# Kernel optimization log

Hardware: AMD Instinct MI355X
Metric: run time of the kernel (lower is better)

The kernel has to match this reference:

```python
import jax, jax.numpy as jnp
import numpy as np

B, F, V, E, A = 4096, 39, 100000, 16, 16


def setup_inputs() -> dict:
    key = jax.random.key(0)
    ks = jax.random.split(key, 9)
    Xi = jax.random.randint(ks[0], (B, F, 1), 0, V, dtype=jnp.int64)
    Xv = jax.random.uniform(ks[1], (B, F), dtype=jnp.float32)
    # stacked per-field embedding tables (all fields share vocab size V)
    emb1 = jax.random.normal(ks[2], (F, V, 1), dtype=jnp.float32) * 0.01   # first-order
    emb2 = jax.random.normal(ks[3], (F, V, E), dtype=jnp.float32) * 0.01   # second-order
    W1 = jax.random.normal(ks[4], (E, A), dtype=jnp.float32) * (1.0 / np.sqrt(E))
    b1 = jnp.zeros((A,), dtype=jnp.float32)
    H = jax.random.normal(ks[5], (A,), dtype=jnp.float32) * 0.2
    Pv = jax.random.normal(ks[6], (E,), dtype=jnp.float32) * 0.2
    bias = jax.random.normal(ks[7], (1,), dtype=jnp.float32) * 0.2
    return {"Xi": Xi, "Xv": Xv, "emb1": emb1, "emb2": emb2,
            "W1": W1, "b1": b1, "H": H, "Pv": Pv, "bias": bias}


def reference(Xi, Xv, emb1, emb2, W1, b1, H, Pv, bias):
    idx = Xi[..., 0]                      # [B, F] (sum over the size-1 index dim is identity)
    f = jnp.arange(idx.shape[1])
    # first-order: per-field scalar embedding * value -> [B, F]
    first = emb1[f[None, :], idx, 0] * Xv
    # second-order: per-field E-dim embedding * value -> [B, F, E]
    second = emb2[f[None, :], idx] * Xv[..., None]
    # pairwise elementwise products e_i * e_j for i<j -> [B, P, E], P = F*(F-1)/2
    ii, jj = np.triu_indices(idx.shape[1], k=1)
    wij = second[:, ii] * second[:, jj]
    # attention scoring (NOTE: source has activation commented out -> pure linear)
    att = jnp.einsum('bpe,ea->bpa', wij, W1) + b1          # [B, P, A]
    scores = jnp.einsum('bpa,a->bp', att, H)               # [B, P]
    attn_w = jax.nn.softmax(scores, axis=1)                # [B, P]
    att_out = jnp.einsum('bpe,e->bp', wij, Pv) * attn_w    # [B, P]
    return bias[0] + first.sum(axis=1) + att_out.sum(axis=1)  # [B]
```

## Files before the change

### kernel.cpp

```cpp
#include <hip/hip_runtime.h>
#include <math.h>


#define BB 4096
#define FF 39
#define VV 100000
#define EE 16
#define AA 16
#define PP (FF * (FF - 1) / 2)
#define SSTRIDE 20

__global__ __launch_bounds__(256) void afm_kernel(
    const int* __restrict__ Xi, const float* __restrict__ Xv,
    const float* __restrict__ emb1, const float* __restrict__ emb2,
    const float* __restrict__ W1, const float* __restrict__ b1,
    const float* __restrict__ H, const float* __restrict__ Pv,
    const float* __restrict__ bias, float* __restrict__ out)
{
    __shared__ float sec[FF * SSTRIDE];
    __shared__ float firstv[64];
    __shared__ float WHs[EE];
    __shared__ float PvS[EE];
    __shared__ short pairtab[PP];
    __shared__ float red[12];
    __shared__ float m_s;

    const int b = blockIdx.x;
    const int t = threadIdx.x;

    if (t < EE) {
        float s = 0.f;
#pragma unroll
        for (int a = 0; a < AA; ++a) s += W1[t * AA + a] * H[a];
        WHs[t] = s;
        PvS[t] = Pv[t];
    }
    if (t >= 64 && t < 128) firstv[t - 64] = 0.f;

    if (t < FF) {
        int base = t * (2 * FF - 1 - t) / 2;
        for (int j = t + 1; j < FF; ++j)
            pairtab[base + (j - t - 1)] = (short)((t << 8) | j);
    }

    if (t < FF * 4) {
        const int f = t >> 2, e4 = t & 3;
        const int idx = Xi[b * FF + f];
        const float xv = Xv[b * FF + f];
        const float4 v = *reinterpret_cast<const float4*>(
            emb2 + ((long)f * VV + idx) * EE + e4 * 4);
        float4 r;
        r.x = v.x * xv; r.y = v.y * xv; r.z = v.z * xv; r.w = v.w * xv;
        *reinterpret_cast<float4*>(&sec[f * SSTRIDE + e4 * 4]) = r;
    }

    if (t >= 192 && t < 192 + FF) {
        const int f = t - 192;
        const int idx = Xi[b * FF + f];
        firstv[f] = emb1[(long)f * VV + idx] * Xv[b * FF + f];
    }

    __syncthreads();

    float wh[EE], pv[EE];
#pragma unroll
    for (int e = 0; e < EE; ++e) { wh[e] = WHs[e]; pv[e] = PvS[e]; }

    float sv[3], qv[3];
    float local_max = -INFINITY;
#pragma unroll
    for (int k = 0; k < 3; ++k) {
        const int p = t + k * 256;
        float s = -INFINITY, q = 0.f;
        if (p < PP) {
            const int ij = pairtab[p];
            const int i = ij >> 8, j = ij & 255;
            const float4* __restrict__ si = reinterpret_cast<const float4*>(&sec[i * SSTRIDE]);
            const float4* __restrict__ sj = reinterpret_cast<const float4*>(&sec[j * SSTRIDE]);
            s = 0.f;
#pragma unroll
            for (int e4 = 0; e4 < 4; ++e4) {
                const float4 a = si[e4];
                const float4 c = sj[e4];
                const float w0 = a.x * c.x, w1 = a.y * c.y, w2 = a.z * c.z, w3 = a.w * c.w;
                s += w0 * wh[e4 * 4 + 0] + w1 * wh[e4 * 4 + 1]
                   + w2 * wh[e4 * 4 + 2] + w3 * wh[e4 * 4 + 3];
                q += w0 * pv[e4 * 4 + 0] + w1 * pv[e4 * 4 + 1]
                   + w2 * pv[e4 * 4 + 2] + w3 * pv[e4 * 4 + 3];
            }
            local_max = fmaxf(local_max, s);
        }
        sv[k] = s; qv[k] = q;
    }

    float m = local_max;
#pragma unroll
    for (int o = 32; o > 0; o >>= 1) m = fmaxf(m, __shfl_xor(m, o, 64));
    const int wid = t >> 6;
    if ((t & 63) == 0) red[wid] = m;
    __syncthreads();
    if (t == 0) m_s = fmaxf(fmaxf(red[0], red[1]), fmaxf(red[2], red[3]));
    __syncthreads();
    m = m_s;

    float den = 0.f, num = 0.f;
#pragma unroll
    for (int k = 0; k < 3; ++k) {
        const float e = __expf(sv[k] - m);
        den += e;
        num += e * qv[k];
    }
    float fs = (t < 64) ? firstv[t] : 0.f;
#pragma unroll
    for (int o = 32; o > 0; o >>= 1) {
        den += __shfl_xor(den, o, 64);
        num += __shfl_xor(num, o, 64);
        fs  += __shfl_xor(fs, o, 64);
    }
    if ((t & 63) == 0) { red[wid] = den; red[4 + wid] = num; red[8 + wid] = fs; }
    __syncthreads();
    if (t == 0) {
        const float D = red[0] + red[1] + red[2] + red[3];
        const float N = red[4] + red[5] + red[6] + red[7];
        out[b] = bias[0] + red[8] + N / D;
    }
}

extern "C" void kernel_launch(void* const* d_in, const int* in_sizes, int n_in,
                              void* d_out, int out_size, void* d_ws, size_t ws_size,
                              hipStream_t stream)
{
    const int*   Xi   = (const int*)d_in[0];
    const float* Xv   = (const float*)d_in[1];
    const float* emb1 = (const float*)d_in[2];
    const float* emb2 = (const float*)d_in[3];
    const float* W1   = (const float*)d_in[4];
    const float* b1   = (const float*)d_in[5];
    const float* H    = (const float*)d_in[6];
    const float* Pv   = (const float*)d_in[7];
    const float* bias = (const float*)d_in[8];
    (void)b1; (void)in_sizes; (void)n_in; (void)out_size; (void)d_ws; (void)ws_size;

    afm_kernel<<<BB, 256, 0, stream>>>(Xi, Xv, emb1, emb2, W1, b1, H, Pv, bias,
                                       (float*)d_out);
}
```

Baseline: 314.2 us.

## Use one wavefront per sample with online softmax over contiguous pair runs

Shrinks each block from 256 threads to a single 64-lane wavefront. Each lane walks 12 consecutive pairs, reusing the premultiplied i-row across j, and keeps an online softmax (running max, denominator, numerator). The partial results are merged with shuffle-only reductions, which removes the shared-memory reduction arrays and all but one barrier. This trades fewer threads per block and less gather parallelism for cheaper reductions and more row reuse. Each lane also does more serial work and uses more registers.

```diff
diff --git a/kernel.cpp b/kernel.cpp
--- a/kernel.cpp
+++ b/kernel.cpp
@@ -1,129 +1,136 @@
 #include <hip/hip_runtime.h>
 #include <math.h>
+#include <float.h>
 
 
 #define BB 4096
 #define FF 39
 #define VV 100000
 #define EE 16
-#define AA 16
-#define PP (FF * (FF - 1) / 2)
-#define SSTRIDE 20
+#define PP 741
+#define SS 20
 
-__global__ __launch_bounds__(256) void afm_kernel(
+__global__ __launch_bounds__(64) void afm_kernel(
     const int* __restrict__ Xi, const float* __restrict__ Xv,
     const float* __restrict__ emb1, const float* __restrict__ emb2,
-    const float* __restrict__ W1, const float* __restrict__ b1,
-    const float* __restrict__ H, const float* __restrict__ Pv,
-    const float* __restrict__ bias, float* __restrict__ out)
+    const float* __restrict__ W1, const float* __restrict__ H,
+    const float* __restrict__ Pv, const float* __restrict__ bias,
+    float* __restrict__ out)
 {
-    __shared__ float sec[FF * SSTRIDE];
-    __shared__ float firstv[64];
-    __shared__ float WHs[EE];
-    __shared__ float PvS[EE];
-    __shared__ short pairtab[PP];
-    __shared__ float red[12];
-    __shared__ float m_s;
+    __shared__ float sec[FF * SS];
 
     const int b = blockIdx.x;
-    const int t = threadIdx.x;
+    const int l = threadIdx.x;
 
-    if (t < EE) {
-        float s = 0.f;
-#pragma unroll
-        for (int a = 0; a < AA; ++a) s += W1[t * AA + a] * H[a];
-        WHs[t] = s;
-        PvS[t] = Pv[t];
-    }
-    if (t >= 64 && t < 128) firstv[t - 64] = 0.f;
-
-    if (t < FF) {
-        int base = t * (2 * FF - 1 - t) / 2;
-        for (int j = t + 1; j < FF; ++j)
-            pairtab[base + (j - t - 1)] = (short)((t << 8) | j);
+    int   xi = 0;
+    float xv = 0.f, fo = 0.f;
+    if (l < FF) {
+        xi = Xi[b * FF + l];
+        xv = Xv[b * FF + l];
+        fo = emb1[(long)l * VV + xi] * xv;
     }
 
-    if (t < FF * 4) {
-        const int f = t >> 2, e4 = t & 3;
-        const int idx = Xi[b * FF + f];
-        const float xv = Xv[b * FF + f];
-        const float4 v = *reinterpret_cast<const float4*>(
-            emb2 + ((long)f * VV + idx) * EE + e4 * 4);
-        float4 r;
-        r.x = v.x * xv; r.y = v.y * xv; r.z = v.z * xv; r.w = v.w * xv;
-        *reinterpret_cast<float4*>(&sec[f * SSTRIDE + e4 * 4]) = r;
+    const int e = l & 15;
+    float whe = 0.f;
+    {
+        const float4* __restrict__ W1r = reinterpret_cast<const float4*>(W1 + e * 16);
+        const float4* __restrict__ H4  = reinterpret_cast<const float4*>(H);
+#pragma unroll
+        for (int m = 0; m < 4; ++m) {
+            const float4 w = W1r[m], h = H4[m];
+            whe += w.x * h.x + w.y * h.y + w.z * h.z + w.w * h.w;
+        }
+    }
+    float wh[16];
+#pragma unroll
+    for (int k = 0; k < 16; ++k) wh[k] = __shfl(whe, k, 64);
+    float pv[16];
+    {
+        const float4* __restrict__ Pv4 = reinterpret_cast<const float4*>(Pv);
+#pragma unroll
+        for (int m = 0; m < 4; ++m) {
+            const float4 v = Pv4[m];
+            pv[m * 4 + 0] = v.x; pv[m * 4 + 1] = v.y;
+            pv[m * 4 + 2] = v.z; pv[m * 4 + 3] = v.w;
+        }
     }
 
-    if (t >= 192 && t < 192 + FF) {
-        const int f = t - 192;
-        const int idx = Xi[b * FF + f];
-        firstv[f] = emb1[(long)f * VV + idx] * Xv[b * FF + f];
+#pragma unroll
+    for (int k = 0; k < 3; ++k) {
+        const int t = l + 64 * k;
+        if (t < FF * 4) {
+            const int f = t >> 2, e4 = t & 3;
+            const int   idxf = __shfl(xi, f, 64);
+            const float xvf  = __shfl(xv, f, 64);
+            float4 v = *reinterpret_cast<const float4*>(
+                emb2 + ((long)f * VV + idxf) * EE + e4 * 4);
+            v.x *= xvf; v.y *= xvf; v.z *= xvf; v.w *= xvf;
+            *reinterpret_cast<float4*>(&sec[f * SS + e4 * 4]) = v;
+        }
+    }
+    __syncthreads();
+
+    const int p0  = l * 12;
+    const int cnt = (PP - p0 < 0) ? 0 : ((PP - p0 < 12) ? (PP - p0) : 12);
+    int rem = (p0 < PP) ? p0 : (PP - 1);
+    int i = 0;
+    while (rem >= FF - 1 - i) { rem -= FF - 1 - i; ++i; }
+    int j = i + 1 + rem;
+
+    float ui[16], ri[16];
+    auto load_i = [&](int ii) {
+#pragma unroll
+        for (int m = 0; m < 4; ++m) {
+            const float4 s4 = *reinterpret_cast<const float4*>(&sec[ii * SS + m * 4]);
+            ui[m * 4 + 0] = s4.x * wh[m * 4 + 0]; ri[m * 4 + 0] = s4.x * pv[m * 4 + 0];
+            ui[m * 4 + 1] = s4.y * wh[m * 4 + 1]; ri[m * 4 + 1] = s4.y * pv[m * 4 + 1];
+            ui[m * 4 + 2] = s4.z * wh[m * 4 + 2]; ri[m * 4 + 2] = s4.z * pv[m * 4 + 2];
+            ui[m * 4 + 3] = s4.w * wh[m * 4 + 3]; ri[m * 4 + 3] = s4.w * pv[m * 4 + 3];
+        }
+    };
+    load_i(i);
+
+    float mx = -FLT_MAX, den = 0.f, num = 0.f;
+#pragma unroll
+    for (int k = 0; k < 12; ++k) {
+        if (k < cnt) {
+            float s = 0.f, q = 0.f;
+#pragma unroll
+            for (int m = 0; m < 4; ++m) {
+                const float4 s4 = *reinterpret_cast<const float4*>(&sec[j * SS + m * 4]);
+                s += ui[m * 4 + 0] * s4.x + ui[m * 4 + 1] * s4.y
+                   + ui[m * 4 + 2] * s4.z + ui[m * 4 + 3] * s4.w;
+                q += ri[m * 4 + 0] * s4.x + ri[m * 4 + 1] * s4.y
+                   + ri[m * 4 + 2] * s4.z + ri[m * 4 + 3] * s4.w;
+            }
+            if (s > mx) {
+                const float sc = __expf(mx - s);
+                den *= sc; num *= sc; mx = s;
+            }
+            const float ex = __expf(s - mx);
+            den += ex;
+            num += ex * q;
+            if (++j == FF) {
+                ++i; j = i + 1;
+                if (k + 1 < cnt) load_i(i);
+            }
+        }
     }
 
-    __syncthreads();
-
-    float wh[EE], pv[EE];
 #pragma unroll
-    for (int e = 0; e < EE; ++e) { wh[e] = WHs[e]; pv[e] = PvS[e]; }
-
-    float sv[3], qv[3];
-    float local_max = -INFINITY;
-#pragma unroll
-    for (int k = 0; k < 3; ++k) {
-        const int p = t + k * 256;
-        float s = -INFINITY, q = 0.f;
-        if (p < PP) {
-            const int ij = pairtab[p];
-            const int i = ij >> 8, j = ij & 255;
-            const float4* __restrict__ si = reinterpret_cast<const float4*>(&sec[i * SSTRIDE]);
-            const float4* __restrict__ sj = reinterpret_cast<const float4*>(&sec[j * SSTRIDE]);
-            s = 0.f;
-#pragma unroll
-            for (int e4 = 0; e4 < 4; ++e4) {
-                const float4 a = si[e4];
-                const float4 c = sj[e4];
-                const float w0 = a.x * c.x, w1 = a.y * c.y, w2 = a.z * c.z, w3 = a.w * c.w;
-                s += w0 * wh[e4 * 4 + 0] + w1 * wh[e4 * 4 + 1]
-                   + w2 * wh[e4 * 4 + 2] + w3 * wh[e4 * 4 + 3];
-                q += w0 * pv[e4 * 4 + 0] + w1 * pv[e4 * 4 + 1]
-                   + w2 * pv[e4 * 4 + 2] + w3 * pv[e4 * 4 + 3];
-            }
-            local_max = fmaxf(local_max, s);
-        }
-        sv[k] = s; qv[k] = q;
+    for (int o = 32; o; o >>= 1) {
+        const float mo = __shfl_xor(mx,  o, 64);
+        const float dl = __shfl_xor(den, o, 64);
+        const float nl = __shfl_xor(num, o, 64);
+        const float mn = fmaxf(mx, mo);
+        const float sa = __expf(mx - mn);
+        const float sb = __expf(mo - mn);
+        den = den * sa + dl * sb;
+        num = num * sa + nl * sb;
+        mx  = mn;
+        fo += __shfl_xor(fo, o, 64);
     }
-
-    float m = local_max;
-#pragma unroll
-    for (int o = 32; o > 0; o >>= 1) m = fmaxf(m, __shfl_xor(m, o, 64));
-    const int wid = t >> 6;
-    if ((t & 63) == 0) red[wid] = m;
-    __syncthreads();
-    if (t == 0) m_s = fmaxf(fmaxf(red[0], red[1]), fmaxf(red[2], red[3]));
-    __syncthreads();
-    m = m_s;
-
-    float den = 0.f, num = 0.f;
-#pragma unroll
-    for (int k = 0; k < 3; ++k) {
-        const float e = __expf(sv[k] - m);
-        den += e;
-        num += e * qv[k];
-    }
-    float fs = (t < 64) ? firstv[t] : 0.f;
-#pragma unroll
-    for (int o = 32; o > 0; o >>= 1) {
-        den += __shfl_xor(den, o, 64);
-        num += __shfl_xor(num, o, 64);
-        fs  += __shfl_xor(fs, o, 64);
-    }
-    if ((t & 63) == 0) { red[wid] = den; red[4 + wid] = num; red[8 + wid] = fs; }
-    __syncthreads();
-    if (t == 0) {
-        const float D = red[0] + red[1] + red[2] + red[3];
-        const float N = red[4] + red[5] + red[6] + red[7];
-        out[b] = bias[0] + red[8] + N / D;
-    }
+    if (l == 0) out[b] = bias[0] + fo + num / den;
 }
 
 extern "C" void kernel_launch(void* const* d_in, const int* in_sizes, int n_in,
@@ -135,12 +142,11 @@
     const float* emb1 = (const float*)d_in[2];
     const float* emb2 = (const float*)d_in[3];
     const float* W1   = (const float*)d_in[4];
-    const float* b1   = (const float*)d_in[5];
     const float* H    = (const float*)d_in[6];
     const float* Pv   = (const float*)d_in[7];
     const float* bias = (const float*)d_in[8];
-    (void)b1; (void)in_sizes; (void)n_in; (void)out_size; (void)d_ws; (void)ws_size;
+    (void)in_sizes; (void)n_in; (void)out_size; (void)d_ws; (void)ws_size;
 
-    afm_kernel<<<BB, 256, 0, stream>>>(Xi, Xv, emb1, emb2, W1, b1, H, Pv, bias,
-                                       (float*)d_out);
+    afm_kernel<<<BB, 64, 0, stream>>>(Xi, Xv, emb1, emb2, W1, H, Pv, bias,
+                                      (float*)d_out);
 }
```

Result: no change. 314.5 us (+0.1%).
